# Performance work log

Hardware: AMD Instinct MI355X
Metric: run time of the kernel (lower is better)

## Reference

```python
import jax, jax.numpy as jnp
import numpy as np

B, N, D = 256, 64, 3
MSG_IN = 3 * D + 2   # [x_i, x_j, r, |r|, |r|^2] = 11
MSG_H = 128
HID = 128


def setup_inputs() -> dict:
    key = jax.random.key(0)
    ks = jax.random.split(key, 16)
    def lin(k, fin, fout):
        k1, k2 = jax.random.split(k)
        lim = 1.0 / np.sqrt(fin)
        w = jax.random.uniform(k1, (fin, fout), jnp.float32, -lim, lim)
        b = jax.random.uniform(k2, (fout,), jnp.float32, -lim, lim)
        return w, b
    phi_w1, phi_b1 = lin(ks[0], MSG_IN, MSG_H)
    phi_w2, phi_b2 = lin(ks[1], MSG_H, MSG_H)
    psi_w1, psi_b1 = lin(ks[2], D + MSG_H, HID)
    psi_w2, psi_b2 = lin(ks[3], HID, HID)
    psi_w3, psi_b3 = lin(ks[4], HID, D)
    x = jax.random.normal(ks[5], (B, N, D), jnp.float32)
    spin = jax.random.randint(ks[6], (N,), 0, 2, jnp.int64 if jax.config.jax_enable_x64 else jnp.int32)
    bf_scale = jnp.float32(0.05)
    return {"x": x, "spin": spin,
            "phi_w1": phi_w1, "phi_b1": phi_b1, "phi_w2": phi_w2, "phi_b2": phi_b2,
            "psi_w1": psi_w1, "psi_b1": psi_b1, "psi_w2": psi_w2, "psi_b2": psi_b2,
            "psi_w3": psi_w3, "psi_b3": psi_b3, "bf_scale": bf_scale}


def reference(x, spin, phi_w1, phi_b1, phi_w2, phi_b2,
              psi_w1, psi_b1, psi_w2, psi_b2, psi_w3, psi_b3, bf_scale):
    b, n, d = x.shape
    r = x[:, :, None, :] - x[:, None, :, :]              # (B,N,N,d)
    r2 = jnp.sum(r * r, axis=-1, keepdims=True)          # (B,N,N,1)
    r1 = jnp.sqrt(r2 + 1e-12)
    xi = jnp.broadcast_to(x[:, :, None, :], (b, n, n, d))
    xj = jnp.broadcast_to(x[:, None, :, :], (b, n, n, d))
    msg_in = jnp.concatenate([xi, xj, r, r1, r2], axis=-1)  # (B,N,N,3d+2)
    # use_spin=True, same_spin_only=False -> mask is all-ones (spin unused)
    eye = jnp.eye(n, dtype=x.dtype)[None, :, :, None]
    mask = 1.0 - eye                                      # zero out self-messages
    h = jax.nn.silu(msg_in @ phi_w1 + phi_b1)
    m_ij = jax.nn.silu(h @ phi_w2 + phi_b2)              # (B,N,N,msg_hidden)
    m_i = jnp.sum(m_ij * mask, axis=2)                   # (B,N,msg_hidden)
    upd = jnp.concatenate([x, m_i], axis=-1)
    u = jax.nn.silu(upd @ psi_w1 + psi_b1)
    u = jax.nn.silu(u @ psi_w2 + psi_b2)
    dx = u @ psi_w3 + psi_b3
    return jnp.tanh(dx) * jnp.maximum(bf_scale, 0.0)
```

## Files before the change

kernel.cpp:

```cpp
#include <hip/hip_runtime.h>
#include <math.h>

#define NT 256

typedef short bf16x8 __attribute__((ext_vector_type(8)));
typedef float f32x4 __attribute__((ext_vector_type(4)));

__device__ __forceinline__ float silu_f(float z) {
    return z / (1.0f + __expf(-z));
}
__device__ __forceinline__ unsigned short f2bf(float f) {
    unsigned int u = __float_as_uint(f);
    u += 0x7FFFu + ((u >> 16) & 1u);
    return (unsigned short)(u >> 16);
}
__device__ __forceinline__ float bf2f(unsigned short s) {
    return __uint_as_float(((unsigned int)s) << 16);
}

__global__ __launch_bounds__(NT, 2) void backflow_kernel(
    const float* __restrict__ x,
    const float* __restrict__ phi_w1, const float* __restrict__ phi_b1,
    const float* __restrict__ phi_w2, const float* __restrict__ phi_b2,
    const float* __restrict__ psi_w1, const float* __restrict__ psi_b1,
    const float* __restrict__ psi_w2, const float* __restrict__ psi_b2,
    const float* __restrict__ psi_w3, const float* __restrict__ psi_b3,
    const float* __restrict__ bf_scale,
    float* __restrict__ out)
{
    __shared__ __align__(16) unsigned short A_hi[64 * 128];
    __shared__ __align__(16) unsigned short A_lo[64 * 128];
    __shared__ __align__(16) float x_l4[64 * 4];
    __shared__ __align__(16) float rf[64 * 8];
    __shared__ __align__(16) float upd_l[8 * 132];
    __shared__ float red_l[48];

    const int tid  = threadIdx.x;
    const int b    = blockIdx.x >> 3;
    const int i0   = (blockIdx.x & 7) * 8;
    const int wv   = tid >> 6;
    const int lane = tid & 63;
    const int lr   = lane & 15;
    const int lg   = lane >> 4;

    bf16x8 bh[2][4], bl[2][4];
    float b2c[2];
    #pragma unroll
    for (int c2 = 0; c2 < 2; ++c2) {
        const int ct = wv + 4 * c2;
        const int n  = ct * 16 + lr;
        b2c[c2] = phi_b2[n];
        #pragma unroll
        for (int ks = 0; ks < 4; ++ks) {
            #pragma unroll
            for (int e = 0; e < 8; ++e) {
                const int k = ks * 32 + lg * 8 + e;
                const float w = phi_w2[k * 128 + n];
                const unsigned short h = f2bf(w);
                bh[c2][ks][e] = (short)h;
                bl[c2][ks][e] = (short)f2bf(w - bf2f(h));
            }
        }
    }

    const int kq = (tid & 31) * 4;
    const int jg = tid >> 5;
    float w1r[44];
    #pragma unroll
    for (int d = 0; d < 11; ++d)
        #pragma unroll
        for (int kk = 0; kk < 4; ++kk)
            w1r[d * 4 + kk] = phi_w1[d * 128 + kq + kk];
    float b1r[4];
    #pragma unroll
    for (int kk = 0; kk < 4; ++kk) b1r[kk] = phi_b1[kq + kk];

    if (tid < 64) {
        x_l4[tid * 4 + 0] = x[b * 192 + tid * 3 + 0];
        x_l4[tid * 4 + 1] = x[b * 192 + tid * 3 + 1];
        x_l4[tid * 4 + 2] = x[b * 192 + tid * 3 + 2];
        x_l4[tid * 4 + 3] = 0.0f;
    }
    __syncthreads();

    #pragma unroll 1
    for (int il = 0; il < 8; ++il) {
        const int i = i0 + il;
        const float xi0 = x_l4[i * 4 + 0], xi1 = x_l4[i * 4 + 1], xi2 = x_l4[i * 4 + 2];

        if (tid < 64) {
            const int j = tid;
            const float4 xj4 = *(const float4*)&x_l4[j * 4];
            const float r0 = xi0 - xj4.x, r1 = xi1 - xj4.y, r2 = xi2 - xj4.z;
            const float r2s = r0 * r0 + r1 * r1 + r2 * r2;
            const float rn  = sqrtf(r2s + 1e-12f);
            float4* p = (float4*)&rf[j * 8];
            p[0] = make_float4(xj4.x, xj4.y, xj4.z, r0);
            p[1] = make_float4(r1, r2, rn, r2s);
        }
        __syncthreads();

        if (tid < 3) upd_l[il * 132 + tid] = x_l4[i * 4 + tid];

        float preb[4];
        #pragma unroll
        for (int kk = 0; kk < 4; ++kk)
            preb[kk] = b1r[kk] + xi0 * w1r[0 + kk] + xi1 * w1r[4 + kk] + xi2 * w1r[8 + kk];

        #pragma unroll
        for (int jj = 0; jj < 8; ++jj) {
            const int j = jg * 8 + jj;
            const float4 f0 = *(const float4*)&rf[j * 8];
            const float4 f1 = *(const float4*)&rf[j * 8 + 4];
            unsigned short hh[4], ll[4];
            #pragma unroll
            for (int kk = 0; kk < 4; ++kk) {
                const float p = preb[kk]
                    + f0.x * w1r[12 + kk] + f0.y * w1r[16 + kk] + f0.z * w1r[20 + kk]
                    + f0.w * w1r[24 + kk] + f1.x * w1r[28 + kk] + f1.y * w1r[32 + kk]
                    + f1.z * w1r[36 + kk] + f1.w * w1r[40 + kk];
                const float h = silu_f(p);
                hh[kk] = f2bf(h);
                ll[kk] = f2bf(h - bf2f(hh[kk]));
            }
            const int byte = ((j * 128 + kq) * 2) ^ ((j & 7) << 4);
            *(ushort4*)((char*)A_hi + byte) = make_ushort4(hh[0], hh[1], hh[2], hh[3]);
            *(ushort4*)((char*)A_lo + byte) = make_ushort4(ll[0], ll[1], ll[2], ll[3]);
        }
        __syncthreads();

        float msum0 = 0.0f, msum1 = 0.0f;
        const int a_base = lr * 256 + lg * 16;
        const int a_swz  = (lr & 7) << 4;
        #pragma unroll
        for (int jt = 0; jt < 4; ++jt) {
            bf16x8 ah[4], al[4];
            #pragma unroll
            for (int ks = 0; ks < 4; ++ks) {
                const int off = (jt * 4096 + ks * 64 + a_base) ^ a_swz;
                ah[ks] = *(const bf16x8*)((const char*)A_hi + off);
                al[ks] = *(const bf16x8*)((const char*)A_lo + off);
            }
            #pragma unroll
            for (int c2 = 0; c2 < 2; ++c2) {
                f32x4 acc = {0.0f, 0.0f, 0.0f, 0.0f};
                #pragma unroll
                for (int ks = 0; ks < 4; ++ks) {
                    acc = __builtin_amdgcn_mfma_f32_16x16x32_bf16(ah[ks], bh[c2][ks], acc, 0, 0, 0);
                    acc = __builtin_amdgcn_mfma_f32_16x16x32_bf16(al[ks], bh[c2][ks], acc, 0, 0, 0);
                    acc = __builtin_amdgcn_mfma_f32_16x16x32_bf16(ah[ks], bl[c2][ks], acc, 0, 0, 0);
                }
                #pragma unroll
                for (int v = 0; v < 4; ++v) {
                    const int row = jt * 16 + lg * 4 + v;
                    const float mv = silu_f(acc[v] + b2c[c2]);
                    const float add = (row == i) ? 0.0f : mv;
                    if (c2 == 0) msum0 += add; else msum1 += add;
                }
            }
        }
        msum0 += __shfl_xor(msum0, 16, 64); msum0 += __shfl_xor(msum0, 32, 64);
        msum1 += __shfl_xor(msum1, 16, 64); msum1 += __shfl_xor(msum1, 32, 64);
        if (lane < 16) {
            upd_l[il * 132 + 3 + (wv) * 16 + lr]     = msum0;
            upd_l[il * 132 + 3 + (wv + 4) * 16 + lr] = msum1;
        }
    }
    __syncthreads();

    float* u1_l = (float*)A_hi;

    const int c   = tid & 127;
    const int rep = tid >> 7;
    const int n0  = rep * 4;
    float a4[4];
    const float pb1 = psi_b1[c];
    #pragma unroll
    for (int nn = 0; nn < 4; ++nn) a4[nn] = pb1;
    #pragma unroll 4
    for (int k = 0; k < 131; ++k) {
        const float w = psi_w1[k * 128 + c];
        #pragma unroll
        for (int nn = 0; nn < 4; ++nn) a4[nn] += upd_l[(n0 + nn) * 132 + k] * w;
    }
    #pragma unroll
    for (int nn = 0; nn < 4; ++nn) u1_l[(n0 + nn) * 132 + c] = silu_f(a4[nn]);
    __syncthreads();

    const float pb2 = psi_b2[c];
    #pragma unroll
    for (int nn = 0; nn < 4; ++nn) a4[nn] = pb2;
    #pragma unroll 4
    for (int k = 0; k < 128; ++k) {
        const float w = psi_w2[k * 128 + c];
        #pragma unroll
        for (int nn = 0; nn < 4; ++nn) a4[nn] += u1_l[(n0 + nn) * 132 + k] * w;
    }
    float u2[4];
    #pragma unroll
    for (int nn = 0; nn < 4; ++nn) u2[nn] = silu_f(a4[nn]);

    const float w30 = psi_w3[c * 3 + 0];
    const float w31 = psi_w3[c * 3 + 1];
    const float w32 = psi_w3[c * 3 + 2];
    float pd[4][3];
    #pragma unroll
    for (int nn = 0; nn < 4; ++nn) {
        pd[nn][0] = u2[nn] * w30;
        pd[nn][1] = u2[nn] * w31;
        pd[nn][2] = u2[nn] * w32;
    }
    #pragma unroll
    for (int off = 32; off > 0; off >>= 1) {
        #pragma unroll
        for (int nn = 0; nn < 4; ++nn) {
            pd[nn][0] += __shfl_xor(pd[nn][0], off, 64);
            pd[nn][1] += __shfl_xor(pd[nn][1], off, 64);
            pd[nn][2] += __shfl_xor(pd[nn][2], off, 64);
        }
    }
    if (lane == 0) {
        #pragma unroll
        for (int nn = 0; nn < 4; ++nn) {
            red_l[wv * 12 + nn * 3 + 0] = pd[nn][0];
            red_l[wv * 12 + nn * 3 + 1] = pd[nn][1];
            red_l[wv * 12 + nn * 3 + 2] = pd[nn][2];
        }
    }
    __syncthreads();
    if (tid < 24) {
        const int n = tid / 3, d = tid % 3;
        const int wa = (n < 4) ? 0 : 2;
        const float dx = red_l[wa * 12 + (n & 3) * 3 + d]
                       + red_l[(wa + 1) * 12 + (n & 3) * 3 + d] + psi_b3[d];
        out[(b * 64 + i0 + n) * 3 + d] = tanhf(dx) * fmaxf(bf_scale[0], 0.0f);
    }
}

extern "C" void kernel_launch(void* const* d_in, const int* in_sizes, int n_in,
                              void* d_out, int out_size, void* d_ws, size_t ws_size,
                              hipStream_t stream) {
    const float* x        = (const float*)d_in[0];
    const float* phi_w1   = (const float*)d_in[2];
    const float* phi_b1   = (const float*)d_in[3];
    const float* phi_w2   = (const float*)d_in[4];
    const float* phi_b2   = (const float*)d_in[5];
    const float* psi_w1   = (const float*)d_in[6];
    const float* psi_b1   = (const float*)d_in[7];
    const float* psi_w2   = (const float*)d_in[8];
    const float* psi_b2   = (const float*)d_in[9];
    const float* psi_w3   = (const float*)d_in[10];
    const float* psi_b3   = (const float*)d_in[11];
    const float* bf_scale = (const float*)d_in[12];
    float* out = (float*)d_out;

    backflow_kernel<<<dim3(2048), dim3(NT), 0, stream>>>(
        x, phi_w1, phi_b1, phi_w2, phi_b2,
        psi_w1, psi_b1, psi_w2, psi_b2, psi_w3, psi_b3,
        bf_scale, out);
}
```

Measured before the change: 258.7 us.

## Compute first message layer with split-bf16 MFMA instead of scalar FMAs

Replaces the per-thread scalar FP32 evaluation of the 11-input first phi layer with bf16 MFMA matrix ops. Both features and weights are split into three bf16 parts, and bias is folded in as a constant-1 feature, to approximate FP32 precision. This moves the 11x128 per-pair FMA work onto matrix cores and frees the 44 weight registers. The cost is extra feature-splitting work, new shared buffers for the packed features, and a small precision risk from dropping the cross terms.

New measurement: 266.0 us. 2.8% more time.

```diff
diff --git a/kernel.cpp b/kernel.cpp
--- a/kernel.cpp
+++ b/kernel.cpp
@@ -16,6 +16,9 @@
 }
 __device__ __forceinline__ float bf2f(unsigned short s) {
     return __uint_as_float(((unsigned int)s) << 16);
+}
+__device__ __forceinline__ unsigned int pk2(unsigned short a, unsigned short b) {
+    return (unsigned int)a | ((unsigned int)b << 16);
 }
 
 __global__ __launch_bounds__(NT, 2) void backflow_kernel(
@@ -30,8 +33,9 @@
 {
     __shared__ __align__(16) unsigned short A_hi[64 * 128];
     __shared__ __align__(16) unsigned short A_lo[64 * 128];
+    __shared__ __align__(16) unsigned char featA1[64 * 80];
+    __shared__ __align__(16) unsigned char featA2[64 * 80];
     __shared__ __align__(16) float x_l4[64 * 4];
-    __shared__ __align__(16) float rf[64 * 8];
     __shared__ __align__(16) float upd_l[8 * 132];
     __shared__ float red_l[48];
 
@@ -63,17 +67,26 @@
         }
     }
 
-    const int kq = (tid & 31) * 4;
-    const int jg = tid >> 5;
-    float w1r[44];
-    #pragma unroll
-    for (int d = 0; d < 11; ++d)
-        #pragma unroll
-        for (int kk = 0; kk < 4; ++kk)
-            w1r[d * 4 + kk] = phi_w1[d * 128 + kq + kk];
-    float b1r[4];
-    #pragma unroll
-    for (int kk = 0; kk < 4; ++kk) b1r[kk] = phi_b1[kq + kk];
+    bf16x8 w1a[2], w1b[2], w1c[2];
+    #pragma unroll
+    for (int c2 = 0; c2 < 2; ++c2) {
+        const int n = (wv + 4 * c2) * 16 + lr;
+        #pragma unroll
+        for (int e = 0; e < 8; ++e) {
+            const int k = lg * 8 + e;
+            const int d = k & 15;
+            float w = 0.0f;
+            if (d <= 10) w = phi_w1[d * 128 + n];
+            else if (d == 11 && k < 16) w = phi_b1[n];
+            const unsigned short hi = f2bf(w);
+            const float rm = w - bf2f(hi);
+            const unsigned short md = f2bf(rm);
+            const unsigned short lo = f2bf(rm - bf2f(md));
+            w1a[c2][e] = (short)hi;
+            w1b[c2][e] = (short)md;
+            w1c[c2][e] = (short)lo;
+        }
+    }
 
     if (tid < 64) {
         x_l4[tid * 4 + 0] = x[b * 192 + tid * 3 + 0];
@@ -86,46 +99,66 @@
     #pragma unroll 1
     for (int il = 0; il < 8; ++il) {
         const int i = i0 + il;
-        const float xi0 = x_l4[i * 4 + 0], xi1 = x_l4[i * 4 + 1], xi2 = x_l4[i * 4 + 2];
 
         if (tid < 64) {
             const int j = tid;
+            const float xi0 = x_l4[i * 4 + 0], xi1 = x_l4[i * 4 + 1], xi2 = x_l4[i * 4 + 2];
             const float4 xj4 = *(const float4*)&x_l4[j * 4];
-            const float r0 = xi0 - xj4.x, r1 = xi1 - xj4.y, r2 = xi2 - xj4.z;
-            const float r2s = r0 * r0 + r1 * r1 + r2 * r2;
-            const float rn  = sqrtf(r2s + 1e-12f);
-            float4* p = (float4*)&rf[j * 8];
-            p[0] = make_float4(xj4.x, xj4.y, xj4.z, r0);
-            p[1] = make_float4(r1, r2, rn, r2s);
+            float F[12];
+            F[0] = xi0; F[1] = xi1; F[2] = xi2;
+            F[3] = xj4.x; F[4] = xj4.y; F[5] = xj4.z;
+            F[6] = xi0 - xj4.x; F[7] = xi1 - xj4.y; F[8] = xi2 - xj4.z;
+            const float r2s = F[6] * F[6] + F[7] * F[7] + F[8] * F[8];
+            F[9]  = sqrtf(r2s + 1e-12f);
+            F[10] = r2s;
+            F[11] = 1.0f;
+            unsigned short fh[12], fm[12], fl[12];
+            #pragma unroll
+            for (int d = 0; d < 12; ++d) {
+                fh[d] = f2bf(F[d]);
+                const float rm = F[d] - bf2f(fh[d]);
+                fm[d] = f2bf(rm);
+                fl[d] = f2bf(rm - bf2f(fm[d]));
+            }
+            uint4* p1 = (uint4*)(featA1 + j * 80);
+            p1[0] = make_uint4(pk2(fh[0], fh[1]), pk2(fh[2], fh[3]), pk2(fh[4], fh[5]), pk2(fh[6], fh[7]));
+            p1[1] = make_uint4(pk2(fh[8], fh[9]), pk2(fh[10], fh[11]), 0u, 0u);
+            p1[2] = make_uint4(pk2(fm[0], fm[1]), pk2(fm[2], fm[3]), pk2(fm[4], fm[5]), pk2(fm[6], fm[7]));
+            p1[3] = make_uint4(pk2(fm[8], fm[9]), pk2(fm[10], 0), 0u, 0u);
+            uint4* p2 = (uint4*)(featA2 + j * 80);
+            p2[0] = make_uint4(pk2(fl[0], fl[1]), pk2(fl[2], fl[3]), pk2(fl[4], fl[5]), pk2(fl[6], fl[7]));
+            p2[1] = make_uint4(pk2(fl[8], fl[9]), pk2(fl[10], 0), 0u, 0u);
+            p2[2] = make_uint4(0u, 0u, 0u, 0u);
+            p2[3] = make_uint4(0u, 0u, 0u, 0u);
         }
         __syncthreads();
 
         if (tid < 3) upd_l[il * 132 + tid] = x_l4[i * 4 + tid];
 
-        float preb[4];
-        #pragma unroll
-        for (int kk = 0; kk < 4; ++kk)
-            preb[kk] = b1r[kk] + xi0 * w1r[0 + kk] + xi1 * w1r[4 + kk] + xi2 * w1r[8 + kk];
-
-        #pragma unroll
-        for (int jj = 0; jj < 8; ++jj) {
-            const int j = jg * 8 + jj;
-            const float4 f0 = *(const float4*)&rf[j * 8];
-            const float4 f1 = *(const float4*)&rf[j * 8 + 4];
-            unsigned short hh[4], ll[4];
-            #pragma unroll
-            for (int kk = 0; kk < 4; ++kk) {
-                const float p = preb[kk]
-                    + f0.x * w1r[12 + kk] + f0.y * w1r[16 + kk] + f0.z * w1r[20 + kk]
-                    + f0.w * w1r[24 + kk] + f1.x * w1r[28 + kk] + f1.y * w1r[32 + kk]
-                    + f1.z * w1r[36 + kk] + f1.w * w1r[40 + kk];
-                const float h = silu_f(p);
-                hh[kk] = f2bf(h);
-                ll[kk] = f2bf(h - bf2f(hh[kk]));
-            }
-            const int byte = ((j * 128 + kq) * 2) ^ ((j & 7) << 4);
-            *(ushort4*)((char*)A_hi + byte) = make_ushort4(hh[0], hh[1], hh[2], hh[3]);
-            *(ushort4*)((char*)A_lo + byte) = make_ushort4(ll[0], ll[1], ll[2], ll[3]);
+        #pragma unroll
+        for (int jt = 0; jt < 4; ++jt) {
+            const int j = jt * 16 + lr;
+            const bf16x8 bf1 = *(const bf16x8*)(featA1 + j * 80 + lg * 16);
+            const bf16x8 bf2v = *(const bf16x8*)(featA2 + j * 80 + lg * 16);
+            #pragma unroll
+            for (int c2 = 0; c2 < 2; ++c2) {
+                f32x4 acc = {0.0f, 0.0f, 0.0f, 0.0f};
+                acc = __builtin_amdgcn_mfma_f32_16x16x32_bf16(w1a[c2], bf1, acc, 0, 0, 0);
+                acc = __builtin_amdgcn_mfma_f32_16x16x32_bf16(w1b[c2], bf1, acc, 0, 0, 0);
+                acc = __builtin_amdgcn_mfma_f32_16x16x32_bf16(w1c[c2], bf1, acc, 0, 0, 0);
+                acc = __builtin_amdgcn_mfma_f32_16x16x32_bf16(w1a[c2], bf2v, acc, 0, 0, 0);
+                unsigned short hh[4], ll[4];
+                #pragma unroll
+                for (int v = 0; v < 4; ++v) {
+                    const float h = silu_f(acc[v]);
+                    hh[v] = f2bf(h);
+                    ll[v] = f2bf(h - bf2f(hh[v]));
+                }
+                const int n0 = (wv + 4 * c2) * 16 + lg * 4;
+                const int byteoff = ((j * 128 + n0) * 2) ^ ((j & 7) << 4);
+                *(ushort4*)((char*)A_hi + byteoff) = make_ushort4(hh[0], hh[1], hh[2], hh[3]);
+                *(ushort4*)((char*)A_lo + byteoff) = make_ushort4(ll[0], ll[1], ll[2], ll[3]);
+            }
         }
         __syncthreads();
 
```

## Use 512-thread blocks covering 16 particles, one MFMA column tile per wave

Applied to the files above, without the earlier changes.

Each block now handles 16 target particles instead of 8, using 512 threads (8 waves), and launches a quarter as many blocks per batch. Each wave now owns a single 16-column slice of the phi second layer instead of two, which halves its preloaded bf16 hi/lo weight registers and its MFMA count per i. The first-layer pair features are spread over twice as many threads. The aim is to spread the per-block weight loading and conversion over more particles and to cut per-wave register use. The cost is fewer blocks overall and larger blocks that must still fit two per CU under the launch bounds.

After: 288.3 us. 1.11x slower.

```diff
diff --git a/kernel.cpp b/kernel.cpp
--- a/kernel.cpp
+++ b/kernel.cpp
@@ -1,7 +1,8 @@
 #include <hip/hip_runtime.h>
 #include <math.h>
 
-#define NT 256
+#define NT 512
+#define GI 16
 
 typedef short bf16x8 __attribute__((ext_vector_type(8)));
 typedef float f32x4 __attribute__((ext_vector_type(4)));
@@ -32,34 +33,28 @@
     __shared__ __align__(16) unsigned short A_lo[64 * 128];
     __shared__ __align__(16) float x_l4[64 * 4];
     __shared__ __align__(16) float rf[64 * 8];
-    __shared__ __align__(16) float upd_l[8 * 132];
-    __shared__ float red_l[48];
+    __shared__ __align__(16) float upd_l[GI * 132];
+    __shared__ float red_l[8 * 12];
 
     const int tid  = threadIdx.x;
-    const int b    = blockIdx.x >> 3;
-    const int i0   = (blockIdx.x & 7) * 8;
+    const int b    = blockIdx.x >> 2;
+    const int i0   = (blockIdx.x & 3) * GI;
     const int wv   = tid >> 6;
     const int lane = tid & 63;
     const int lr   = lane & 15;
     const int lg   = lane >> 4;
 
-    bf16x8 bh[2][4], bl[2][4];
-    float b2c[2];
-    #pragma unroll
-    for (int c2 = 0; c2 < 2; ++c2) {
-        const int ct = wv + 4 * c2;
-        const int n  = ct * 16 + lr;
-        b2c[c2] = phi_b2[n];
-        #pragma unroll
-        for (int ks = 0; ks < 4; ++ks) {
-            #pragma unroll
-            for (int e = 0; e < 8; ++e) {
-                const int k = ks * 32 + lg * 8 + e;
-                const float w = phi_w2[k * 128 + n];
-                const unsigned short h = f2bf(w);
-                bh[c2][ks][e] = (short)h;
-                bl[c2][ks][e] = (short)f2bf(w - bf2f(h));
-            }
+    bf16x8 bh[4], bl[4];
+    const float b2c = phi_b2[wv * 16 + lr];
+    #pragma unroll
+    for (int ks = 0; ks < 4; ++ks) {
+        #pragma unroll
+        for (int e = 0; e < 8; ++e) {
+            const int k = ks * 32 + lg * 8 + e;
+            const float w = phi_w2[k * 128 + wv * 16 + lr];
+            const unsigned short h = f2bf(w);
+            bh[ks][e] = (short)h;
+            bl[ks][e] = (short)f2bf(w - bf2f(h));
         }
     }
 
@@ -84,7 +79,7 @@
     __syncthreads();
 
     #pragma unroll 1
-    for (int il = 0; il < 8; ++il) {
+    for (int il = 0; il < GI; ++il) {
         const int i = i0 + il;
         const float xi0 = x_l4[i * 4 + 0], xi1 = x_l4[i * 4 + 1], xi2 = x_l4[i * 4 + 2];
 
@@ -108,8 +103,8 @@
             preb[kk] = b1r[kk] + xi0 * w1r[0 + kk] + xi1 * w1r[4 + kk] + xi2 * w1r[8 + kk];
 
         #pragma unroll
-        for (int jj = 0; jj < 8; ++jj) {
-            const int j = jg * 8 + jj;
+        for (int jj = 0; jj < 4; ++jj) {
+            const int j = jg * 4 + jj;
             const float4 f0 = *(const float4*)&rf[j * 8];
             const float4 f1 = *(const float4*)&rf[j * 8 + 4];
             unsigned short hh[4], ll[4];
@@ -129,7 +124,7 @@
         }
         __syncthreads();
 
-        float msum0 = 0.0f, msum1 = 0.0f;
+        float msum = 0.0f;
         const int a_base = lr * 256 + lg * 16;
         const int a_swz  = (lr & 7) << 4;
         #pragma unroll
@@ -141,30 +136,23 @@
                 ah[ks] = *(const bf16x8*)((const char*)A_hi + off);
                 al[ks] = *(const bf16x8*)((const char*)A_lo + off);
             }
-            #pragma unroll
-            for (int c2 = 0; c2 < 2; ++c2) {
-                f32x4 acc = {0.0f, 0.0f, 0.0f, 0.0f};
-                #pragma unroll
-                for (int ks = 0; ks < 4; ++ks) {
-                    acc = __builtin_amdgcn_mfma_f32_16x16x32_bf16(ah[ks], bh[c2][ks], acc, 0, 0, 0);
-                    acc = __builtin_amdgcn_mfma_f32_16x16x32_bf16(al[ks], bh[c2][ks], acc, 0, 0, 0);
-                    acc = __builtin_amdgcn_mfma_f32_16x16x32_bf16(ah[ks], bl[c2][ks], acc, 0, 0, 0);
-                }
-                #pragma unroll
-                for (int v = 0; v < 4; ++v) {
-                    const int row = jt * 16 + lg * 4 + v;
-                    const float mv = silu_f(acc[v] + b2c[c2]);
-                    const float add = (row == i) ? 0.0f : mv;
-                    if (c2 == 0) msum0 += add; else msum1 += add;
-                }
-            }
-        }
-        msum0 += __shfl_xor(msum0, 16, 64); msum0 += __shfl_xor(msum0, 32, 64);
-        msum1 += __shfl_xor(msum1, 16, 64); msum1 += __shfl_xor(msum1, 32, 64);
-        if (lane < 16) {
-            upd_l[il * 132 + 3 + (wv) * 16 + lr]     = msum0;
-            upd_l[il * 132 + 3 + (wv + 4) * 16 + lr] = msum1;
-        }
+            f32x4 acc = {0.0f, 0.0f, 0.0f, 0.0f};
+            #pragma unroll
+            for (int ks = 0; ks < 4; ++ks) {
+                acc = __builtin_amdgcn_mfma_f32_16x16x32_bf16(ah[ks], bh[ks], acc, 0, 0, 0);
+                acc = __builtin_amdgcn_mfma_f32_16x16x32_bf16(al[ks], bh[ks], acc, 0, 0, 0);
+                acc = __builtin_amdgcn_mfma_f32_16x16x32_bf16(ah[ks], bl[ks], acc, 0, 0, 0);
+            }
+            #pragma unroll
+            for (int v = 0; v < 4; ++v) {
+                const int row = jt * 16 + lg * 4 + v;
+                const float mv = silu_f(acc[v] + b2c);
+                msum += (row == i) ? 0.0f : mv;
+            }
+        }
+        msum += __shfl_xor(msum, 16, 64);
+        msum += __shfl_xor(msum, 32, 64);
+        if (lane < 16) upd_l[il * 132 + 3 + wv * 16 + lr] = msum;
     }
     __syncthreads();
 
@@ -228,11 +216,11 @@
         }
     }
     __syncthreads();
-    if (tid < 24) {
+    if (tid < GI * 3) {
         const int n = tid / 3, d = tid % 3;
-        const int wa = (n < 4) ? 0 : 2;
-        const float dx = red_l[wa * 12 + (n & 3) * 3 + d]
-                       + red_l[(wa + 1) * 12 + (n & 3) * 3 + d] + psi_b3[d];
+        const int r = n >> 2, nn = n & 3;
+        const float dx = red_l[(2 * r) * 12 + nn * 3 + d]
+                       + red_l[(2 * r + 1) * 12 + nn * 3 + d] + psi_b3[d];
         out[(b * 64 + i0 + n) * 3 + d] = tanhf(dx) * fmaxf(bf_scale[0], 0.0f);
     }
 }
@@ -254,7 +242,7 @@
     const float* bf_scale = (const float*)d_in[12];
     float* out = (float*)d_out;
 
-    backflow_kernel<<<dim3(2048), dim3(NT), 0, stream>>>(
+    backflow_kernel<<<dim3(256 * (64 / GI)), dim3(NT), 0, stream>>>(
         x, phi_w1, phi_b1, phi_w2, phi_b2,
         psi_w1, psi_b1, psi_w2, psi_b2, psi_w3, psi_b3,
         bf_scale, out);
```
